# Performance work log

Hardware: AMD Instinct MI355X
Metric: run time of the kernel (lower is better)

Reference implementation:

```python
import jax, jax.numpy as jnp
import numpy as np

N_NODES = 100000
MAX_DEG = 16
D_IN = 256
D_OUT = 256


def setup_inputs() -> dict:
    key = jax.random.key(0)
    k1, k2, k3, k4, k5 = jax.random.split(key, 5)
    x = jax.random.normal(k1, (N_NODES, D_IN), dtype=jnp.float32)
    # padded edge list: -1 marks padding; first column always valid so degree >= 1
    col0 = jax.random.randint(k2, (N_NODES, 1), 0, N_NODES)
    rest = jax.random.randint(k3, (N_NODES, MAX_DEG - 1), -1, N_NODES)
    edge_index = jnp.concatenate([col0, rest], axis=1).astype(jnp.int64)
    # torch Linear(2*D_IN, D_OUT): weight [D_OUT, 2*D_IN], bias [D_OUT]
    W = jax.random.normal(k4, (D_OUT, 2 * D_IN), dtype=jnp.float32) * 0.05
    b = jax.random.normal(k5, (D_OUT,), dtype=jnp.float32) * 0.05
    return {"x": x, "edge_index": edge_index, "W": W, "b": b}


def reference(x, edge_index, W, b):
    # pad with a zero row so index -1 (padding) gathers zeros, matching torch
    padded = jnp.concatenate([x, jnp.zeros((1, x.shape[1]), dtype=x.dtype)], axis=0)
    neigh = padded[edge_index]  # [N, MAX_DEG, D_IN]
    degree = jnp.sum(edge_index >= 0, axis=-1, keepdims=True).astype(x.dtype)  # [N, 1]
    neigh_agg = jnp.sum(neigh, axis=1) / degree  # mean aggregation, [N, D_IN]
    h = jnp.concatenate([x, neigh_agg], axis=1)  # [N, 2*D_IN]
    return h @ W.T + b
```

## Files before the change

### kernel.cpp

```cpp
#include <hip/hip_runtime.h>
#include <stdint.h>


#define MAX_DEG 16
#define D_IN 256
#define D_OUT 256
#define N_NODES_C 100000
#define BM 64

typedef __attribute__((ext_vector_type(8))) short bf16x8;
typedef __attribute__((ext_vector_type(4))) float f32x4;

typedef const __attribute__((address_space(1))) void* gas_ptr;
typedef __attribute__((address_space(3))) void* las_ptr;

__device__ __forceinline__ uint32_t f2bf(float f) {
    union { float f; uint32_t u; } v; v.f = f;
    uint32_t u = v.u;
    return (u + 0x7FFFu + ((u >> 16) & 1u)) >> 16;
}
__device__ __forceinline__ uint32_t pack2(float lo, float hi) {
    return f2bf(lo) | (f2bf(hi) << 16);
}

__global__ __launch_bounds__(256) void cast_w2f_kernel(
    const float* __restrict__ W, ushort* __restrict__ Wb2f, ushort* __restrict__ y2)
{
    if (blockIdx.x < 64) {
        const int t = blockIdx.x * 256 + threadIdx.x;
        const int cg   = t >> 9;
        const int ks   = (t >> 6) & 7;
        const int lane = t & 63;
        const int quad = lane >> 4, r16 = lane & 15;
        const int c = cg * 16 + r16;
        const int k = ks * 32 + quad * 8;
        const float* src = W + (size_t)(c & 255) * 512 + (c >> 8) * 256 + k;
        float4 v0 = ((const float4*)src)[0];
        float4 v1 = ((const float4*)src)[1];
        uint4 p = { pack2(v0.x, v0.y), pack2(v0.z, v0.w),
                    pack2(v1.x, v1.y), pack2(v1.z, v1.w) };
        *(uint4*)(Wb2f + (size_t)t * 8) = p;
    } else {
        if (threadIdx.x < 32) {
            uint4 z = {0u, 0u, 0u, 0u};
            *(uint4*)(y2 + (size_t)N_NODES_C * 256 + threadIdx.x * 8) = z;
        }
    }
}

__global__ __launch_bounds__(512, 4) void gemm_xw_kernel(
    const float* __restrict__ x, const ushort* __restrict__ Wb2f,
    const float* __restrict__ bias, ushort* __restrict__ y2,
    float* __restrict__ out)
{
    __shared__ float sX[BM * 256];

    const int tid = threadIdx.x;
    const int node0 = blockIdx.x * BM;
    const int w = tid >> 6;
    const int lane = tid & 63;

    #pragma unroll
    for (int it = 0; it < 8; ++it) {
        const int R = w * 8 + it;
        const int rg = node0 + R;
        const float* rowp = x + (size_t)(rg < N_NODES_C ? rg : N_NODES_C - 1) * D_IN;
        const char* gsrc = (const char*)rowp + ((lane ^ it) << 4);
        __builtin_amdgcn_global_load_lds((gas_ptr)gsrc,
            (las_ptr)((char*)sX + (size_t)R * 1024), 16, 0, 0);
    }
    __syncthreads();

    const int quad = lane >> 4;
    const int r16  = lane & 15;
    const int x7   = r16 & 7;

    f32x4 acc[4][4];
    #pragma unroll
    for (int s = 0; s < 4; ++s)
        #pragma unroll
        for (int j = 0; j < 4; ++j)
            acc[s][j] = (f32x4){0.f, 0.f, 0.f, 0.f};

    const char* aB[4];
    #pragma unroll
    for (int s = 0; s < 4; ++s)
        aB[s] = (const char*)sX + (size_t)(s * 16 + r16) * 1024;
    const ushort* bp = Wb2f + ((size_t)(w * 4) * 8 + 0) * 64 * 8 + lane * 8;

    #pragma unroll
    for (int ks = 0; ks < D_IN / 32; ++ks) {
        const int ch = ks * 8 + quad * 2;
        bf16x8 afr[4];
        #pragma unroll
        for (int s = 0; s < 4; ++s) {
            f32x4 lo = *(const f32x4*)(aB[s] + ((ch ^ x7) << 4));
            f32x4 hi = *(const f32x4*)(aB[s] + (((ch + 1) ^ x7) << 4));
            union { uint32_t u[4]; bf16x8 v; } cv;
            cv.u[0] = pack2(lo.x, lo.y);
            cv.u[1] = pack2(lo.z, lo.w);
            cv.u[2] = pack2(hi.x, hi.y);
            cv.u[3] = pack2(hi.z, hi.w);
            afr[s] = cv.v;
        }
        #pragma unroll
        for (int j = 0; j < 4; ++j) {
            bf16x8 b = *(const bf16x8*)(bp + ((size_t)j * 8 + ks) * 64 * 8);
            acc[0][j] = __builtin_amdgcn_mfma_f32_16x16x32_bf16(afr[0], b, acc[0][j], 0, 0, 0);
            acc[1][j] = __builtin_amdgcn_mfma_f32_16x16x32_bf16(afr[1], b, acc[1][j], 0, 0, 0);
            acc[2][j] = __builtin_amdgcn_mfma_f32_16x16x32_bf16(afr[2], b, acc[2][j], 0, 0, 0);
            acc[3][j] = __builtin_amdgcn_mfma_f32_16x16x32_bf16(afr[3], b, acc[3][j], 0, 0, 0);
        }
    }

    if (w < 4) {
        #pragma unroll
        for (int j = 0; j < 4; ++j) {
            const int c = w * 64 + j * 16 + r16;
            const float bv = bias[c];
            #pragma unroll
            for (int s = 0; s < 4; ++s)
                #pragma unroll
                for (int r = 0; r < 4; ++r) {
                    const int row = node0 + s * 16 + quad * 4 + r;
                    if (row < N_NODES_C)
                        ((ushort*)(out + (size_t)row * D_OUT))[c] =
                            (ushort)f2bf(acc[s][j][r] + bv);
                }
        }
    } else {
        #pragma unroll
        for (int j = 0; j < 4; ++j) {
            const int c2 = (w - 4) * 64 + j * 16 + r16;
            #pragma unroll
            for (int s = 0; s < 4; ++s)
                #pragma unroll
                for (int r = 0; r < 4; ++r) {
                    const int row = node0 + s * 16 + quad * 4 + r;
                    if (row < N_NODES_C)
                        y2[(size_t)row * 256 + c2] = (ushort)f2bf(acc[s][j][r]);
                }
        }
    }
}

__global__ __launch_bounds__(256, 5) void gather_add_kernel(
    const ushort* __restrict__ y2, const int* __restrict__ edge,
    float* __restrict__ out)
{
    __shared__ char sBuf[4 * 8 * 1024];

    const int w4   = threadIdx.x >> 6;
    const int lane = threadIdx.x & 63;
    const int i = blockIdx.x * 4 + w4;

    const int e = edge[(size_t)i * MAX_DEG + (lane & 15)];
    const unsigned long long vm = __ballot(e >= 0);
    const int deg = (int)__popcll(vm & 0xFFFFull);
    const float inv = 1.0f / (float)deg;

    const uint32_t off_me = (uint32_t)(e < 0 ? N_NODES_C : e) * 512u;
    const char* yb = (const char*)y2;
    const uint32_t coff = (uint32_t)((lane & 31) * 16);
    const int half = lane >> 5;

    const int cw = (lane & 31) * 8 + half * 4;
    float* op = out + (size_t)i * D_OUT + cw;
    const uint2 y1p = *(const uint2*)((const char*)(out + (size_t)i * D_OUT) + cw * 2);

    char* lw = sBuf + (size_t)w4 * 8192;
    #pragma unroll
    for (int k = 0; k < 8; ++k) {
        const uint32_t ro = (uint32_t)__shfl((int)off_me, 2 * k + half, 64);
        const char* gsrc = yb + (size_t)(ro + coff);
        __builtin_amdgcn_global_load_lds((gas_ptr)gsrc, (las_ptr)(lw + k * 1024),
                                         16, 0, 0);
    }
    asm volatile("s_waitcnt vmcnt(0)" ::: "memory");
    __builtin_amdgcn_sched_barrier(0);

    float a[8];
    #pragma unroll
    for (int q = 0; q < 8; ++q) a[q] = 0.f;
    #pragma unroll
    for (int k = 0; k < 8; ++k) {
        uint4 g = *(const uint4*)(lw + k * 1024 + lane * 16);
        uint32_t u[4] = { g.x, g.y, g.z, g.w };
        #pragma unroll
        for (int q = 0; q < 4; ++q) {
            union { uint32_t ui; float f; } lo, hi;
            lo.ui = u[q] << 16;
            hi.ui = u[q] & 0xFFFF0000u;
            a[2*q]   += lo.f;
            a[2*q+1] += hi.f;
        }
    }
    #pragma unroll
    for (int q = 0; q < 8; ++q) a[q] += __shfl_xor(a[q], 32, 64);

    const int q0 = half * 4;
    union { uint32_t ui; float f; } c0, c1, c2, c3;
    c0.ui = y1p.x << 16; c1.ui = y1p.x & 0xFFFF0000u;
    c2.ui = y1p.y << 16; c3.ui = y1p.y & 0xFFFF0000u;
    float4 r;
    r.x = c0.f + inv * a[q0 + 0];
    r.y = c1.f + inv * a[q0 + 1];
    r.z = c2.f + inv * a[q0 + 2];
    r.w = c3.f + inv * a[q0 + 3];
    *(float4*)op = r;
}

#define D_K 512
#define LDS_STRIDE 520

__global__ __launch_bounds__(256) void cast_w_kernel(const float* __restrict__ W,
                                                     ushort* __restrict__ Wb) {
    int i = (blockIdx.x * 256 + threadIdx.x) * 4;
    float4 v = *(const float4*)(W + i);
    ushort4 p = { (ushort)f2bf(v.x), (ushort)f2bf(v.y),
                  (ushort)f2bf(v.z), (ushort)f2bf(v.w) };
    *(ushort4*)(Wb + i) = p;
}

__global__ __launch_bounds__(256) void sage_fp32_kernel(
    const float* __restrict__ x, const int* __restrict__ edge,
    const ushort* __restrict__ Wb, const float* __restrict__ bias,
    float* __restrict__ out)
{
    __shared__ ushort sH[32 * LDS_STRIDE];
    const int tid = threadIdx.x;
    const int node0 = blockIdx.x * 32;
    {
        const int m = tid >> 3, l = tid & 7;
        const int node = node0 + m;
        const float4* xrow = (const float4*)(x + (size_t)node * D_IN);
        ushort* dst = sH + m * LDS_STRIDE + l * 32;
        #pragma unroll
        for (int q = 0; q < 8; ++q) {
            float4 v = xrow[l * 8 + q];
            ushort4 p = { (ushort)f2bf(v.x), (ushort)f2bf(v.y),
                          (ushort)f2bf(v.z), (ushort)f2bf(v.w) };
            *(ushort4*)(dst + q * 4) = p;
        }
        float4 agg[8];
        #pragma unroll
        for (int q = 0; q < 8; ++q) agg[q] = make_float4(0.f,0.f,0.f,0.f);
        int deg = 0;
        for (int d = 0; d < MAX_DEG; ++d) {
            int nb = edge[(size_t)node * MAX_DEG + d];
            if (nb >= 0) {
                ++deg;
                const float4* nr = (const float4*)(x + (size_t)nb * D_IN);
                #pragma unroll
                for (int q = 0; q < 8; ++q) {
                    float4 t = nr[l * 8 + q];
                    agg[q].x += t.x; agg[q].y += t.y;
                    agg[q].z += t.z; agg[q].w += t.w;
                }
            }
        }
        const float inv = 1.0f / (float)deg;
        ushort* dst2 = sH + m * LDS_STRIDE + D_IN + l * 32;
        #pragma unroll
        for (int q = 0; q < 8; ++q) {
            ushort4 p = { (ushort)f2bf(agg[q].x*inv), (ushort)f2bf(agg[q].y*inv),
                          (ushort)f2bf(agg[q].z*inv), (ushort)f2bf(agg[q].w*inv) };
            *(ushort4*)(dst2 + q * 4) = p;
        }
    }
    __syncthreads();
    {
        const int wave = tid >> 6, lane = tid & 63;
        const int quad = lane >> 4, r16 = lane & 15;
        const int mt = wave & 1, nh = wave >> 1;
        f32x4 acc[8];
        #pragma unroll
        for (int j = 0; j < 8; ++j) {
            float bv = bias[(nh * 8 + j) * 16 + r16];
            acc[j] = (f32x4){bv, bv, bv, bv};
        }
        const ushort* arow = sH + (mt * 16 + r16) * LDS_STRIDE + quad * 8;
        #pragma unroll
        for (int ks = 0; ks < D_K / 32; ++ks) {
            bf16x8 a = *(const bf16x8*)(arow + ks * 32);
            #pragma unroll
            for (int j = 0; j < 8; ++j) {
                const int o = (nh * 8 + j) * 16 + r16;
                bf16x8 b = *(const bf16x8*)(Wb + (size_t)o * D_K + ks * 32 + quad * 8);
                acc[j] = __builtin_amdgcn_mfma_f32_16x16x32_bf16(a, b, acc[j], 0, 0, 0);
            }
        }
        #pragma unroll
        for (int j = 0; j < 8; ++j) {
            const int o = (nh * 8 + j) * 16 + r16;
            #pragma unroll
            for (int r = 0; r < 4; ++r) {
                const int row = node0 + mt * 16 + quad * 4 + r;
                out[(size_t)row * D_OUT + o] = acc[j][r];
            }
        }
    }
}

extern "C" void kernel_launch(void* const* d_in, const int* in_sizes, int n_in,
                              void* d_out, int out_size, void* d_ws, size_t ws_size,
                              hipStream_t stream) {
    const float* x    = (const float*)d_in[0];
    const int*   edge = (const int*)d_in[1];
    const float* W    = (const float*)d_in[2];
    const float* bias = (const float*)d_in[3];
    float* out = (float*)d_out;

    const size_t y2_bytes = (size_t)(N_NODES_C + 1) * 256 * 2;
    const size_t wb_bytes = (size_t)512 * 256 * 2;
    const int n = in_sizes[0] / D_IN;

    if (ws_size >= y2_bytes + wb_bytes) {
        ushort* y2   = (ushort*)d_ws;
        ushort* Wb2f = (ushort*)((char*)d_ws + y2_bytes);
        cast_w2f_kernel<<<65, 256, 0, stream>>>(W, Wb2f, y2);
        gemm_xw_kernel<<<(n + BM - 1) / BM, 512, 0, stream>>>(x, Wb2f, bias, y2, out);
        gather_add_kernel<<<n / 4, 256, 0, stream>>>(y2, edge, out);
    } else {
        ushort* Wb = (ushort*)d_ws;
        cast_w_kernel<<<(D_OUT * D_K) / 1024, 256, 0, stream>>>(W, Wb);
        sage_fp32_kernel<<<n / 32, 256, 0, stream>>>(x, edge, Wb, bias, out);
    }
}
```

Measured before the change: 373.7 us.

## Stage GEMM epilogue through LDS for coalesced stores and prefetch B fragments

Replaces scattered 2-byte global stores in the GEMM epilogue with a swizzled LDS staging buffer, then writes rows out as coalesced 16-byte stores. It also double-buffers the B fragment loads one k-step ahead, pinning them in registers with empty asm, and hoists the bias load ahead of the barrier. Occupancy bound drops from 4 to 2 blocks per SM to allow more registers. The trade is extra barriers and LDS traffic plus lower occupancy.

```diff
diff --git a/kernel.cpp b/kernel.cpp
--- a/kernel.cpp
+++ b/kernel.cpp
@@ -48,7 +48,18 @@
     }
 }
 
-__global__ __launch_bounds__(512, 4) void gemm_xw_kernel(
+#define PINB4(b0, b1, b2, b3) do {                                          \
+    const uint4& u0 = *(const uint4*)&(b0);                                 \
+    const uint4& u1 = *(const uint4*)&(b1);                                 \
+    const uint4& u2 = *(const uint4*)&(b2);                                 \
+    const uint4& u3 = *(const uint4*)&(b3);                                 \
+    asm volatile("" :: "v"(u0.x), "v"(u0.y), "v"(u0.z), "v"(u0.w),          \
+                       "v"(u1.x), "v"(u1.y), "v"(u1.z), "v"(u1.w),          \
+                       "v"(u2.x), "v"(u2.y), "v"(u2.z), "v"(u2.w),          \
+                       "v"(u3.x), "v"(u3.y), "v"(u3.z), "v"(u3.w));         \
+} while (0)
+
+__global__ __launch_bounds__(512, 2) void gemm_xw_kernel(
     const float* __restrict__ x, const ushort* __restrict__ Wb2f,
     const float* __restrict__ bias, ushort* __restrict__ y2,
     float* __restrict__ out)
@@ -69,11 +80,18 @@
         __builtin_amdgcn_global_load_lds((gas_ptr)gsrc,
             (las_ptr)((char*)sX + (size_t)R * 1024), 16, 0, 0);
     }
-    __syncthreads();
 
     const int quad = lane >> 4;
     const int r16  = lane & 15;
     const int x7   = r16 & 7;
+    const int cb   = (w & 3) * 64;
+
+    float bv[4];
+    #pragma unroll
+    for (int j = 0; j < 4; ++j)
+        bv[j] = bias[cb + j * 16 + r16];
+
+    __syncthreads();
 
     f32x4 acc[4][4];
     #pragma unroll
@@ -88,8 +106,20 @@
         aB[s] = (const char*)sX + (size_t)(s * 16 + r16) * 1024;
     const ushort* bp = Wb2f + ((size_t)(w * 4) * 8 + 0) * 64 * 8 + lane * 8;
 
+    bf16x8 bcur[4], bnxt[4];
+    #pragma unroll
+    for (int j = 0; j < 4; ++j)
+        bcur[j] = *(const bf16x8*)(bp + ((size_t)j * 8 + 0) * 64 * 8);
+    PINB4(bcur[0], bcur[1], bcur[2], bcur[3]);
+
     #pragma unroll
     for (int ks = 0; ks < D_IN / 32; ++ks) {
+        if (ks < D_IN / 32 - 1) {
+            #pragma unroll
+            for (int j = 0; j < 4; ++j)
+                bnxt[j] = *(const bf16x8*)(bp + ((size_t)j * 8 + ks + 1) * 64 * 8);
+            PINB4(bnxt[0], bnxt[1], bnxt[2], bnxt[3]);
+        }
         const int ch = ks * 8 + quad * 2;
         bf16x8 afr[4];
         #pragma unroll
@@ -105,41 +135,53 @@
         }
         #pragma unroll
         for (int j = 0; j < 4; ++j) {
-            bf16x8 b = *(const bf16x8*)(bp + ((size_t)j * 8 + ks) * 64 * 8);
-            acc[0][j] = __builtin_amdgcn_mfma_f32_16x16x32_bf16(afr[0], b, acc[0][j], 0, 0, 0);
-            acc[1][j] = __builtin_amdgcn_mfma_f32_16x16x32_bf16(afr[1], b, acc[1][j], 0, 0, 0);
-            acc[2][j] = __builtin_amdgcn_mfma_f32_16x16x32_bf16(afr[2], b, acc[2][j], 0, 0, 0);
-            acc[3][j] = __builtin_amdgcn_mfma_f32_16x16x32_bf16(afr[3], b, acc[3][j], 0, 0, 0);
-        }
-    }
-
-    if (w < 4) {
+            acc[0][j] = __builtin_amdgcn_mfma_f32_16x16x32_bf16(afr[0], bcur[j], acc[0][j], 0, 0, 0);
+            acc[1][j] = __builtin_amdgcn_mfma_f32_16x16x32_bf16(afr[1], bcur[j], acc[1][j], 0, 0, 0);
+            acc[2][j] = __builtin_amdgcn_mfma_f32_16x16x32_bf16(afr[2], bcur[j], acc[2][j], 0, 0, 0);
+            acc[3][j] = __builtin_amdgcn_mfma_f32_16x16x32_bf16(afr[3], bcur[j], acc[3][j], 0, 0, 0);
+        }
+        #pragma unroll
+        for (int j = 0; j < 4; ++j) bcur[j] = bnxt[j];
+    }
+
+    __syncthreads();
+    {
+        ushort* sE = (ushort*)sX;
+        const int reg_ = (w < 4) ? 0 : 1;
         #pragma unroll
         for (int j = 0; j < 4; ++j) {
-            const int c = w * 64 + j * 16 + r16;
-            const float bv = bias[c];
+            const int c = cb + j * 16 + r16;
             #pragma unroll
             for (int s = 0; s < 4; ++s)
                 #pragma unroll
                 for (int r = 0; r < 4; ++r) {
-                    const int row = node0 + s * 16 + quad * 4 + r;
-                    if (row < N_NODES_C)
-                        ((ushort*)(out + (size_t)row * D_OUT))[c] =
-                            (ushort)f2bf(acc[s][j][r] + bv);
+                    const int row = s * 16 + quad * 4 + r;
+                    const float v = acc[s][j][r] + (reg_ ? 0.f : bv[j]);
+                    const int a = reg_ * 16384 + row * 256 +
+                                  ((((c >> 3) ^ (row & 7)) << 3) | (c & 7));
+                    sE[a] = (ushort)f2bf(v);
                 }
         }
-    } else {
-        #pragma unroll
-        for (int j = 0; j < 4; ++j) {
-            const int c2 = (w - 4) * 64 + j * 16 + r16;
-            #pragma unroll
-            for (int s = 0; s < 4; ++s)
-                #pragma unroll
-                for (int r = 0; r < 4; ++r) {
-                    const int row = node0 + s * 16 + quad * 4 + r;
-                    if (row < N_NODES_C)
-                        y2[(size_t)row * 256 + c2] = (ushort)f2bf(acc[s][j][r]);
-                }
+    }
+    __syncthreads();
+    {
+        const ushort* sE = (const ushort*)sX;
+        #pragma unroll
+        for (int t = 0; t < 8; ++t) {
+            const int idx = t * 512 + tid;
+            const int reg_ = idx >> 11;
+            const int rowch = idx & 2047;
+            const int row = rowch >> 5;
+            const int ch  = rowch & 31;
+            const int rg = node0 + row;
+            if (rg < N_NODES_C) {
+                const uint4 v = *(const uint4*)(sE + reg_ * 16384 + row * 256 +
+                                                ((ch ^ (row & 7)) << 3));
+                char* dst = reg_ == 0
+                    ? (char*)(out + (size_t)rg * D_OUT) + ch * 16
+                    : (char*)y2 + (size_t)rg * 512 + ch * 16;
+                *(uint4*)dst = v;
+            }
         }
     }
 }
```

Result: faster. 361.4 us (-3.3%).
